# Performance work log

Measured on AMD Instinct MI355X. Metric: run time of the kernel, lower is better.

## Reference

```python
import jax, jax.numpy as jnp
import numpy as np

N = 50000          # nodes
E = 1600000        # edges
IN_C = 128
HID = 128
OUT_C = 1
NUM_LAYERS = 3     # extra conv2 applications
NUM_GRAPHS = 128


def setup_inputs() -> dict:
    key = jax.random.key(0)
    ks = jax.random.split(key, 10)
    x = jax.random.normal(ks[0], (N, IN_C), dtype=jnp.float32)
    edge_index = jax.random.randint(ks[1], (2, E), 0, N, dtype=jnp.int64)
    batch = jnp.sort(jax.random.randint(ks[2], (N,), 0, NUM_GRAPHS, dtype=jnp.int64))
    s1 = 1.0 / np.sqrt(IN_C)
    s2 = 1.0 / np.sqrt(HID)
    W1 = jax.random.uniform(ks[3], (IN_C, HID), jnp.float32, -s1, s1)
    b1 = jnp.zeros((HID,), jnp.float32)
    W2 = jax.random.uniform(ks[4], (HID, HID), jnp.float32, -s2, s2)
    b2 = jnp.zeros((HID,), jnp.float32)
    Wfc = jax.random.uniform(ks[5], (HID, OUT_C), jnp.float32, -s2, s2)
    bfc = jnp.zeros((OUT_C,), jnp.float32)
    return {"x": x, "edge_index": edge_index, "batch": batch,
            "W1": W1, "b1": b1, "W2": W2, "b2": b2, "Wfc": Wfc, "bfc": bfc}


def _gcn_conv(x, W, b, src, dst, dinv):
    # GCNConv: h = X W; out[i] = sum_{j->i} h[j]/sqrt(d_j d_i) + h[i]/d_i + b
    # (self-loops added, symmetric degree normalization, deg includes self-loop)
    h = x @ W                                   # [N, out]
    coef = dinv[src] * dinv[dst]                # [E]
    agg = jax.ops.segment_sum(h[src] * coef[:, None], dst, num_segments=N)
    agg = agg + h * (dinv * dinv)[:, None]      # self-loop contribution
    return agg + b


def reference(x, edge_index, batch, W1, b1, W2, b2, Wfc, bfc):
    src, dst = edge_index[0], edge_index[1]
    # degree of target nodes, +1 for self-loop
    deg = jax.ops.segment_sum(jnp.ones((E,), x.dtype), dst, num_segments=N) + 1.0
    dinv = jax.lax.rsqrt(deg)

    h = jax.nn.relu(_gcn_conv(x, W1, b1, src, dst, dinv))
    for _ in range(NUM_LAYERS):
        h = jax.nn.relu(_gcn_conv(h, W2, b2, src, dst, dinv))
    # dropout is identity here (eval / deterministic reference)

    # global_mean_pool over graphs in the batch
    sums = jax.ops.segment_sum(h, batch, num_segments=NUM_GRAPHS)
    counts = jax.ops.segment_sum(jnp.ones((N,), h.dtype), batch, num_segments=NUM_GRAPHS)
    pooled = sums / jnp.clip(counts, 1.0)[:, None]   # [G, HID]
    return pooled @ Wfc + bfc                        # [G, OUT_C]
```

## Files before the change

### kernel.cpp

```cpp
#include <hip/hip_runtime.h>
#include <hip/hip_bf16.h>


__global__ void count_deg_kernel(const int* __restrict__ dst, int* __restrict__ deg, int E) {
    int i = blockIdx.x * blockDim.x + threadIdx.x;
    int e = i * 4;
    if (e + 3 < E) {
        int4 d = *(const int4*)(dst + e);
        atomicAdd(&deg[d.x], 1);
        atomicAdd(&deg[d.y], 1);
        atomicAdd(&deg[d.z], 1);
        atomicAdd(&deg[d.w], 1);
    } else {
        for (; e < E; e++) atomicAdd(&deg[dst[e]], 1);
    }
}

__global__ void dinv_kernel(const int* __restrict__ deg, float* __restrict__ dinv,
                            float* __restrict__ h0, float* __restrict__ h1,
                            int n, int ns) {
    int i = blockIdx.x * blockDim.x + threadIdx.x;
    if (i < n) dinv[i] = (float)(1.0 / sqrt((double)(deg[i] + 1)));
    if (i < 128) {
        int p = i >> 5, c = i & 31;
        size_t off = (size_t)p * ns * 32 + (size_t)n * 32 + c;
        h0[off] = 0.f;
        h1[off] = 0.f;
    }
}

__global__ void scan_blocksum_kernel(const int* __restrict__ cnt, int* __restrict__ bsum,
                                     int n2) {
    __shared__ int red[256];
    int t = threadIdx.x;
    int i = blockIdx.x * 256 + t;
    red[t] = (i < n2) ? cnt[i] : 0;
    __syncthreads();
    for (int off = 128; off > 0; off >>= 1) {
        if (t < off) red[t] += red[t + off];
        __syncthreads();
    }
    if (t == 0) bsum[blockIdx.x] = red[0];
}

__global__ __launch_bounds__(1024) void scan_bsum_kernel(const int* __restrict__ bsum,
                                                         int* __restrict__ boff, int nb) {
    __shared__ int s[1024];
    int t = threadIdx.x;
    int v = (t < nb) ? bsum[t] : 0;
    s[t] = v;
    __syncthreads();
    for (int off = 1; off < 1024; off <<= 1) {
        int u = (t >= off) ? s[t - off] : 0;
        __syncthreads();
        s[t] += u;
        __syncthreads();
    }
    if (t < nb) boff[t] = s[t] - v;
}

__global__ void scan_final_kernel(const int* __restrict__ cnt, const int* __restrict__ boff,
                                  int* __restrict__ row, int n2) {
    __shared__ int s[256];
    int t = threadIdx.x;
    int b = blockIdx.x;
    int i = b * 256 + t;
    int v = (i < n2) ? cnt[i] : 0;
    s[t] = v;
    __syncthreads();
    for (int off = 1; off < 256; off <<= 1) {
        int u = (t >= off) ? s[t - off] : 0;
        __syncthreads();
        s[t] += u;
        __syncthreads();
    }
    int incl = s[t];
    int base = boff[b];
    if (i < n2) row[i] = base + incl - v;
    if (i == n2 - 1) row[n2] = base + incl;
}

__global__ __launch_bounds__(256) void csr_fill_kernel(const int* __restrict__ src,
                                                       const int* __restrict__ dst,
                                                       const int* __restrict__ row,
                                                       int* __restrict__ fill,
                                                       unsigned short* __restrict__ csr,
                                                       int E, int N) {
    int g  = blockIdx.x & 7;
    int gb = blockIdx.x >> 3;
    int group_blocks = gridDim.x >> 3;
    int R  = (N + 7) >> 3;
    int lo = g * R;
    int hi = lo + R; if (hi > N) hi = N;

    int tig    = gb * blockDim.x + threadIdx.x;
    int stride = group_blocks * blockDim.x;
    int nq = (E + 3) >> 2;

    for (int q = tig; q < nq; q += stride) {
        int e = q * 4;
        if (e + 3 < E) {
            int4 d = *(const int4*)(dst + e);
            if (d.x >= lo && d.x < hi) {
                int pos = row[d.x] + atomicAdd(&fill[d.x], 1);
                csr[pos] = (unsigned short)src[e + 0];
            }
            if (d.y >= lo && d.y < hi) {
                int pos = row[d.y] + atomicAdd(&fill[d.y], 1);
                csr[pos] = (unsigned short)src[e + 1];
            }
            if (d.z >= lo && d.z < hi) {
                int pos = row[d.z] + atomicAdd(&fill[d.z], 1);
                csr[pos] = (unsigned short)src[e + 2];
            }
            if (d.w >= lo && d.w < hi) {
                int pos = row[d.w] + atomicAdd(&fill[d.w], 1);
                csr[pos] = (unsigned short)src[e + 3];
            }
        } else {
            for (; e < E; e++) {
                int d = dst[e];
                if (d >= lo && d < hi) {
                    int pos = row[d] + atomicAdd(&fill[d], 1);
                    csr[pos] = (unsigned short)src[e];
                }
            }
        }
    }
}

__global__ __launch_bounds__(256) void gemm_kernel(const float* __restrict__ A,
                                                   const float* __restrict__ W,
                                                   const float* __restrict__ dinv,
                                                   float* __restrict__ C, int n, int ns,
                                                   int a_blocked) {
    __shared__ float sW[2][16 * 128];
    __shared__ float sA[2][16 * 68];
    int t = threadIdx.x;
    int row0 = blockIdx.x * 64;

    int a_rowi = t >> 2;
    int a_q    = t & 3;
    int w_krow = t >> 4;
    int w_c    = (t & 15) * 8;

    auto a_src = [&](int kb) -> const float* {
        int rr = row0 + a_rowi; if (rr > n - 1) rr = n - 1;
        return a_blocked
            ? (A + ((size_t)(kb >> 1) * ns + rr) * 32 + (kb & 1) * 16 + a_q * 4)
            : (A + (size_t)rr * 128 + kb * 16 + a_q * 4);
    };

    {
        float4 av = *(const float4*)a_src(0);
        float4 w0 = *(const float4*)(W + (size_t)w_krow * 128 + w_c);
        float4 w1 = *(const float4*)(W + (size_t)w_krow * 128 + w_c + 4);
        sA[0][(a_q * 4 + 0) * 68 + a_rowi] = av.x;
        sA[0][(a_q * 4 + 1) * 68 + a_rowi] = av.y;
        sA[0][(a_q * 4 + 2) * 68 + a_rowi] = av.z;
        sA[0][(a_q * 4 + 3) * 68 + a_rowi] = av.w;
        *(float4*)(&sW[0][w_krow * 128 + w_c])     = w0;
        *(float4*)(&sW[0][w_krow * 128 + w_c + 4]) = w1;
    }
    __syncthreads();

    int rg = t >> 4;
    int cg = (t & 15) * 8;

    float acc[4][8];
    #pragma unroll
    for (int j = 0; j < 4; j++)
        #pragma unroll
        for (int c = 0; c < 8; c++) acc[j][c] = 0.f;

    #pragma unroll 1
    for (int kb = 0; kb < 8; kb++) {
        float4 pa, pw0, pw1;
        if (kb < 7) {
            pa  = *(const float4*)a_src(kb + 1);
            pw0 = *(const float4*)(W + (size_t)((kb + 1) * 16 + w_krow) * 128 + w_c);
            pw1 = *(const float4*)(W + (size_t)((kb + 1) * 16 + w_krow) * 128 + w_c + 4);
        }

        const float* ab = sA[kb & 1];
        const float* wb = sW[kb & 1];
        #pragma unroll
        for (int k = 0; k < 16; k++) {
            float4 a4 = *(const float4*)(ab + k * 68 + rg * 4);
            float4 w0 = *(const float4*)(wb + k * 128 + cg);
            float4 w1 = *(const float4*)(wb + k * 128 + cg + 4);
            #pragma unroll
            for (int j = 0; j < 4; j++) {
                float av = (j == 0) ? a4.x : (j == 1) ? a4.y : (j == 2) ? a4.z : a4.w;
                acc[j][0] = fmaf(av, w0.x, acc[j][0]);
                acc[j][1] = fmaf(av, w0.y, acc[j][1]);
                acc[j][2] = fmaf(av, w0.z, acc[j][2]);
                acc[j][3] = fmaf(av, w0.w, acc[j][3]);
                acc[j][4] = fmaf(av, w1.x, acc[j][4]);
                acc[j][5] = fmaf(av, w1.y, acc[j][5]);
                acc[j][6] = fmaf(av, w1.z, acc[j][6]);
                acc[j][7] = fmaf(av, w1.w, acc[j][7]);
            }
        }

        if (kb < 7) {
            int nb = (kb + 1) & 1;
            sA[nb][(a_q * 4 + 0) * 68 + a_rowi] = pa.x;
            sA[nb][(a_q * 4 + 1) * 68 + a_rowi] = pa.y;
            sA[nb][(a_q * 4 + 2) * 68 + a_rowi] = pa.z;
            sA[nb][(a_q * 4 + 3) * 68 + a_rowi] = pa.w;
            *(float4*)(&sW[nb][w_krow * 128 + w_c])     = pw0;
            *(float4*)(&sW[nb][w_krow * 128 + w_c + 4]) = pw1;
        }
        __syncthreads();
    }

    int p  = cg >> 5;
    int cw = cg & 31;
    float* Cb = C + (size_t)p * ns * 32 + cw;
    #pragma unroll
    for (int j = 0; j < 4; j++) {
        int rr = row0 + rg * 4 + j;
        if (rr < n) {
            float dsc = dinv[rr];
            *(float4*)(Cb + (size_t)rr * 32) =
                make_float4(acc[j][0] * dsc, acc[j][1] * dsc,
                            acc[j][2] * dsc, acc[j][3] * dsc);
            *(float4*)(Cb + (size_t)rr * 32 + 4) =
                make_float4(acc[j][4] * dsc, acc[j][5] * dsc,
                            acc[j][6] * dsc, acc[j][7] * dsc);
        }
    }
}

__global__ __launch_bounds__(256) void agg_kernel(const float* __restrict__ h,
                                                  const int* __restrict__ row_ptr,
                                                  const unsigned short* __restrict__ csr,
                                                  const float* __restrict__ dinv,
                                                  const float* __restrict__ bias,
                                                  float* __restrict__ out,
                                                  int n, int ns) {
    int p = blockIdx.x & 3;
    int i = (blockIdx.x >> 2) * 32 + (threadIdx.x >> 3);
    int q = threadIdx.x & 7;
    bool valid = (i < n);
    int iv = valid ? i : 0;

    const float* slice  = h   + (size_t)p * ns * 32;
    float*       oslice = out + (size_t)p * ns * 32;

    int beg = row_ptr[iv];
    int end = valid ? row_ptr[iv + 1] : beg;
    int qoff = q << 2;

    float di = dinv[iv];
    float4 self = *(const float4*)(slice + ((size_t)iv << 5) + qoff);
    float4 b4   = *(const float4*)(bias + p * 32 + qoff);

    float4 acc = make_float4(0.f, 0.f, 0.f, 0.f);

    int e = beg;
    int s0 = (int)__builtin_nontemporal_load(csr + e);
    int s1 = (int)__builtin_nontemporal_load(csr + e + 1);
    int s2 = (int)__builtin_nontemporal_load(csr + e + 2);
    int s3 = (int)__builtin_nontemporal_load(csr + e + 3);
    int s4 = (int)__builtin_nontemporal_load(csr + e + 4);
    int s5 = (int)__builtin_nontemporal_load(csr + e + 5);
    int s6 = (int)__builtin_nontemporal_load(csr + e + 6);
    int s7 = (int)__builtin_nontemporal_load(csr + e + 7);

    while (__any(e < end)) {
        int en = e + 8;
        int t0 = (int)__builtin_nontemporal_load(csr + en);
        int t1 = (int)__builtin_nontemporal_load(csr + en + 1);
        int t2 = (int)__builtin_nontemporal_load(csr + en + 2);
        int t3 = (int)__builtin_nontemporal_load(csr + en + 3);
        int t4 = (int)__builtin_nontemporal_load(csr + en + 4);
        int t5 = (int)__builtin_nontemporal_load(csr + en + 5);
        int t6 = (int)__builtin_nontemporal_load(csr + en + 6);
        int t7 = (int)__builtin_nontemporal_load(csr + en + 7);

        int g0 = (e     < end) ? s0 : n;
        int g1 = (e + 1 < end) ? s1 : n;
        int g2 = (e + 2 < end) ? s2 : n;
        int g3 = (e + 3 < end) ? s3 : n;
        int g4 = (e + 4 < end) ? s4 : n;
        int g5 = (e + 5 < end) ? s5 : n;
        int g6 = (e + 6 < end) ? s6 : n;
        int g7 = (e + 7 < end) ? s7 : n;

        float4 v0 = *(const float4*)(slice + ((size_t)g0 << 5) + qoff);
        float4 v1 = *(const float4*)(slice + ((size_t)g1 << 5) + qoff);
        float4 v2 = *(const float4*)(slice + ((size_t)g2 << 5) + qoff);
        float4 v3 = *(const float4*)(slice + ((size_t)g3 << 5) + qoff);
        float4 v4 = *(const float4*)(slice + ((size_t)g4 << 5) + qoff);
        float4 v5 = *(const float4*)(slice + ((size_t)g5 << 5) + qoff);
        float4 v6 = *(const float4*)(slice + ((size_t)g6 << 5) + qoff);
        float4 v7 = *(const float4*)(slice + ((size_t)g7 << 5) + qoff);

        acc.x += v0.x; acc.y += v0.y; acc.z += v0.z; acc.w += v0.w;
        acc.x += v1.x; acc.y += v1.y; acc.z += v1.z; acc.w += v1.w;
        acc.x += v2.x; acc.y += v2.y; acc.z += v2.z; acc.w += v2.w;
        acc.x += v3.x; acc.y += v3.y; acc.z += v3.z; acc.w += v3.w;
        acc.x += v4.x; acc.y += v4.y; acc.z += v4.z; acc.w += v4.w;
        acc.x += v5.x; acc.y += v5.y; acc.z += v5.z; acc.w += v5.w;
        acc.x += v6.x; acc.y += v6.y; acc.z += v6.z; acc.w += v6.w;
        acc.x += v7.x; acc.y += v7.y; acc.z += v7.z; acc.w += v7.w;

        e = en;
        s0 = t0; s1 = t1; s2 = t2; s3 = t3;
        s4 = t4; s5 = t5; s6 = t6; s7 = t7;
    }

    if (valid) {
        float4 o;
        o.x = fmaxf(fmaf(acc.x + self.x, di, b4.x), 0.f);
        o.y = fmaxf(fmaf(acc.y + self.y, di, b4.y), 0.f);
        o.z = fmaxf(fmaf(acc.z + self.z, di, b4.z), 0.f);
        o.w = fmaxf(fmaf(acc.w + self.w, di, b4.w), 0.f);
        *(float4*)(oslice + ((size_t)i << 5) + qoff) = o;
    }
}

__global__ __launch_bounds__(128) void pool_partial_kernel(const float* __restrict__ h,
                                                           const int* __restrict__ batch,
                                                           double* __restrict__ partials,
                                                           int n, int ns, int S) {
    int g = blockIdx.x / S;
    int s = blockIdx.x % S;
    int c = threadIdx.x;
    const float* hb = h + (size_t)(c >> 5) * ns * 32 + (c & 31);

    int lo = 0, hi = n;
    while (lo < hi) { int mid = (lo + hi) >> 1; if (batch[mid] < g) lo = mid + 1; else hi = mid; }
    int start = lo;
    lo = start; hi = n;
    while (lo < hi) { int mid = (lo + hi) >> 1; if (batch[mid] < g + 1) lo = mid + 1; else hi = mid; }
    int end = lo;

    int cnt = end - start;
    int per = (cnt + S - 1) / S;
    int rs = start + s * per;
    int re = rs + per; if (re > end) re = end;

    double a0 = 0.0, a1 = 0.0, a2 = 0.0, a3 = 0.0;
    int r = rs;
    for (; r + 4 <= re; r += 4) {
        a0 += (double)hb[(size_t)(r + 0) * 32];
        a1 += (double)hb[(size_t)(r + 1) * 32];
        a2 += (double)hb[(size_t)(r + 2) * 32];
        a3 += (double)hb[(size_t)(r + 3) * 32];
    }
    for (; r < re; r++) a0 += (double)hb[(size_t)r * 32];
    partials[(size_t)(g * S + s) * 128 + c] = (a0 + a1) + (a2 + a3);
}

__global__ __launch_bounds__(128) void pool_fc_final_kernel(const double* __restrict__ partials,
                                                            const int* __restrict__ batch,
                                                            const float* __restrict__ Wfc,
                                                            const float* __restrict__ bfc,
                                                            float* __restrict__ out,
                                                            int n, int S) {
    int g = blockIdx.x;
    int c = threadIdx.x;

    int lo = 0, hi = n;
    while (lo < hi) { int mid = (lo + hi) >> 1; if (batch[mid] < g) lo = mid + 1; else hi = mid; }
    int start = lo;
    lo = start; hi = n;
    while (lo < hi) { int mid = (lo + hi) >> 1; if (batch[mid] < g + 1) lo = mid + 1; else hi = mid; }
    int cnt = lo - start;

    double sum = 0.0;
    for (int s = 0; s < S; s++) sum += partials[(size_t)(g * S + s) * 128 + c];
    double mean = sum / (double)(cnt > 0 ? cnt : 1);
    double v = mean * (double)Wfc[c];

    __shared__ double red[128];
    red[c] = v;
    __syncthreads();
    for (int off = 64; off > 0; off >>= 1) {
        if (c < off) red[c] += red[c + off];
        __syncthreads();
    }
    if (c == 0) out[g] = (float)(red[0] + (double)bfc[0]);
}

extern "C" void kernel_launch(void* const* d_in, const int* in_sizes, int n_in,
                              void* d_out, int out_size, void* d_ws, size_t ws_size,
                              hipStream_t stream) {
    const float* x          = (const float*)d_in[0];
    const int*   edge_index = (const int*)d_in[1];
    const int*   batch      = (const int*)d_in[2];
    const float* W1  = (const float*)d_in[3];
    const float* b1  = (const float*)d_in[4];
    const float* W2  = (const float*)d_in[5];
    const float* b2  = (const float*)d_in[6];
    const float* Wfc = (const float*)d_in[7];
    const float* bfc = (const float*)d_in[8];
    float* out = (float*)d_out;

    const int N = in_sizes[2];
    const int E = in_sizes[1] / 2;
    const int G = out_size;
    const int NS = N + 1;

    const int* e_src = edge_index;
    const int* e_dst = edge_index + E;

    char* p = (char*)d_ws;
    auto alloc = [&](size_t bytes) {
        void* r = (void*)p;
        p += (bytes + 255) & ~(size_t)255;
        return r;
    };
    const int S = 8;
    const int NB = (N + 255) / 256;
    float*          h0        = (float*)alloc((size_t)NS * 128 * 4);
    float*          h1        = (float*)alloc((size_t)NS * 128 * 4);
    unsigned short* csr       = (unsigned short*)alloc(((size_t)E + 1024) * 2);
    int*            row       = (int*)  alloc((size_t)(N + 1) * 4);
    int*            deg       = (int*)  alloc((size_t)N * 4);
    int*            fill      = (int*)  alloc((size_t)N * 4);
    int*            bsum      = (int*)  alloc((size_t)NB * 4);
    int*            boff      = (int*)  alloc((size_t)NB * 4);
    float*          dinv      = (float*)alloc((size_t)N * 4);
    double*         partials  = (double*)alloc((size_t)G * S * 128 * 8);
    (void)ws_size; (void)n_in;

    hipMemsetAsync(deg,  0, (size_t)N * 4, stream);
    hipMemsetAsync(fill, 0, (size_t)N * 4, stream);

    int tb = 256;
    int e4 = (E + 3) / 4;
    count_deg_kernel<<<(e4 + tb - 1) / tb, tb, 0, stream>>>(e_dst, deg, E);
    dinv_kernel<<<(N + tb - 1) / tb, tb, 0, stream>>>(deg, dinv, h0, h1, N, NS);
    scan_blocksum_kernel<<<NB, 256, 0, stream>>>(deg, bsum, N);
    scan_bsum_kernel<<<1, 1024, 0, stream>>>(bsum, boff, NB);
    scan_final_kernel<<<NB, 256, 0, stream>>>(deg, boff, row, N);
    csr_fill_kernel<<<1024, tb, 0, stream>>>(e_src, e_dst, row, fill, csr, E, N);

    int gemm_blocks = (N + 63) / 64;
    int agg_blocks  = 4 * ((N + 31) / 32);

    gemm_kernel<<<gemm_blocks, 256, 0, stream>>>(x, W1, dinv, h1, N, NS, 0);
    agg_kernel<<<agg_blocks, 256, 0, stream>>>(h1, row, csr, dinv, b1, h0, N, NS);

    for (int l = 0; l < 3; l++) {
        gemm_kernel<<<gemm_blocks, 256, 0, stream>>>(h0, W2, dinv, h1, N, NS, 1);
        agg_kernel<<<agg_blocks, 256, 0, stream>>>(h1, row, csr, dinv, b2, h0, N, NS);
    }

    pool_partial_kernel<<<G * S, 128, 0, stream>>>(h0, batch, partials, N, NS, S);
    pool_fc_final_kernel<<<G, 128, 0, stream>>>(partials, batch, Wfc, bfc, out, N, S);
}
```

Measured before the change: 711.0 us.

## Record per-edge slot from degree atomics, build CSR without second atomic pass

The degree-count kernel now keeps the value returned by each atomicAdd as the edge's slot within its destination row. The CSR fill becomes a plain scatter with no atomics and no 8-way range partitioning, and the fill buffer and its memset are dropped. The dinv computation and padding-row zeroing move into the scan kernel, removing one launch. Aggregation output now uses nontemporal stores. The cost is an extra E-sized position array that is written and read once, and the CSR order within each row is still nondeterministic.

```diff
diff --git a/kernel.cpp b/kernel.cpp
--- a/kernel.cpp
+++ b/kernel.cpp
@@ -2,30 +2,21 @@
 #include <hip/hip_bf16.h>
 
 
-__global__ void count_deg_kernel(const int* __restrict__ dst, int* __restrict__ deg, int E) {
+typedef float nfloat4 __attribute__((ext_vector_type(4)));
+
+__global__ void count_deg_kernel(const int* __restrict__ dst, int* __restrict__ deg,
+                                 int* __restrict__ pos, int E) {
     int i = blockIdx.x * blockDim.x + threadIdx.x;
     int e = i * 4;
     if (e + 3 < E) {
         int4 d = *(const int4*)(dst + e);
-        atomicAdd(&deg[d.x], 1);
-        atomicAdd(&deg[d.y], 1);
-        atomicAdd(&deg[d.z], 1);
-        atomicAdd(&deg[d.w], 1);
+        int p0 = atomicAdd(&deg[d.x], 1);
+        int p1 = atomicAdd(&deg[d.y], 1);
+        int p2 = atomicAdd(&deg[d.z], 1);
+        int p3 = atomicAdd(&deg[d.w], 1);
+        *(int4*)(pos + e) = make_int4(p0, p1, p2, p3);
     } else {
-        for (; e < E; e++) atomicAdd(&deg[dst[e]], 1);
-    }
-}
-
-__global__ void dinv_kernel(const int* __restrict__ deg, float* __restrict__ dinv,
-                            float* __restrict__ h0, float* __restrict__ h1,
-                            int n, int ns) {
-    int i = blockIdx.x * blockDim.x + threadIdx.x;
-    if (i < n) dinv[i] = (float)(1.0 / sqrt((double)(deg[i] + 1)));
-    if (i < 128) {
-        int p = i >> 5, c = i & 31;
-        size_t off = (size_t)p * ns * 32 + (size_t)n * 32 + c;
-        h0[off] = 0.f;
-        h1[off] = 0.f;
+        for (; e < E; e++) pos[e] = atomicAdd(&deg[dst[e]], 1);
     }
 }
 
@@ -60,7 +51,9 @@
 }
 
 __global__ void scan_final_kernel(const int* __restrict__ cnt, const int* __restrict__ boff,
-                                  int* __restrict__ row, int n2) {
+                                  int* __restrict__ row, float* __restrict__ dinv,
+                                  float* __restrict__ h0, float* __restrict__ h1,
+                                  int n2, int ns) {
     __shared__ int s[256];
     int t = threadIdx.x;
     int b = blockIdx.x;
@@ -76,56 +69,37 @@
     }
     int incl = s[t];
     int base = boff[b];
-    if (i < n2) row[i] = base + incl - v;
+    if (i < n2) {
+        row[i] = base + incl - v;
+        dinv[i] = (float)(1.0 / sqrt((double)(v + 1)));
+    }
     if (i == n2 - 1) row[n2] = base + incl;
+    if (i < 128) {
+        int p = i >> 5, c = i & 31;
+        size_t off2 = (size_t)p * ns * 32 + (size_t)n2 * 32 + c;
+        h0[off2] = 0.f;
+        h1[off2] = 0.f;
+    }
 }
 
 __global__ __launch_bounds__(256) void csr_fill_kernel(const int* __restrict__ src,
                                                        const int* __restrict__ dst,
                                                        const int* __restrict__ row,
-                                                       int* __restrict__ fill,
+                                                       const int* __restrict__ pos,
                                                        unsigned short* __restrict__ csr,
-                                                       int E, int N) {
-    int g  = blockIdx.x & 7;
-    int gb = blockIdx.x >> 3;
-    int group_blocks = gridDim.x >> 3;
-    int R  = (N + 7) >> 3;
-    int lo = g * R;
-    int hi = lo + R; if (hi > N) hi = N;
-
-    int tig    = gb * blockDim.x + threadIdx.x;
-    int stride = group_blocks * blockDim.x;
-    int nq = (E + 3) >> 2;
-
-    for (int q = tig; q < nq; q += stride) {
-        int e = q * 4;
-        if (e + 3 < E) {
-            int4 d = *(const int4*)(dst + e);
-            if (d.x >= lo && d.x < hi) {
-                int pos = row[d.x] + atomicAdd(&fill[d.x], 1);
-                csr[pos] = (unsigned short)src[e + 0];
-            }
-            if (d.y >= lo && d.y < hi) {
-                int pos = row[d.y] + atomicAdd(&fill[d.y], 1);
-                csr[pos] = (unsigned short)src[e + 1];
-            }
-            if (d.z >= lo && d.z < hi) {
-                int pos = row[d.z] + atomicAdd(&fill[d.z], 1);
-                csr[pos] = (unsigned short)src[e + 2];
-            }
-            if (d.w >= lo && d.w < hi) {
-                int pos = row[d.w] + atomicAdd(&fill[d.w], 1);
-                csr[pos] = (unsigned short)src[e + 3];
-            }
-        } else {
-            for (; e < E; e++) {
-                int d = dst[e];
-                if (d >= lo && d < hi) {
-                    int pos = row[d] + atomicAdd(&fill[d], 1);
-                    csr[pos] = (unsigned short)src[e];
-                }
-            }
-        }
+                                                       int E) {
+    int i = blockIdx.x * blockDim.x + threadIdx.x;
+    int e = i * 4;
+    if (e + 3 < E) {
+        int4 d = *(const int4*)(dst + e);
+        int4 s = *(const int4*)(src + e);
+        int4 p = *(const int4*)(pos + e);
+        csr[row[d.x] + p.x] = (unsigned short)s.x;
+        csr[row[d.y] + p.y] = (unsigned short)s.y;
+        csr[row[d.z] + p.z] = (unsigned short)s.z;
+        csr[row[d.w] + p.w] = (unsigned short)s.w;
+    } else {
+        for (; e < E; e++) csr[row[dst[e]] + pos[e]] = (unsigned short)src[e];
     }
 }
 
@@ -313,12 +287,12 @@
     }
 
     if (valid) {
-        float4 o;
+        nfloat4 o;
         o.x = fmaxf(fmaf(acc.x + self.x, di, b4.x), 0.f);
         o.y = fmaxf(fmaf(acc.y + self.y, di, b4.y), 0.f);
         o.z = fmaxf(fmaf(acc.z + self.z, di, b4.z), 0.f);
         o.w = fmaxf(fmaf(acc.w + self.w, di, b4.w), 0.f);
-        *(float4*)(oslice + ((size_t)i << 5) + qoff) = o;
+        __builtin_nontemporal_store(o, (nfloat4*)(oslice + ((size_t)i << 5) + qoff));
     }
 }
 
@@ -421,24 +395,22 @@
     unsigned short* csr       = (unsigned short*)alloc(((size_t)E + 1024) * 2);
     int*            row       = (int*)  alloc((size_t)(N + 1) * 4);
     int*            deg       = (int*)  alloc((size_t)N * 4);
-    int*            fill      = (int*)  alloc((size_t)N * 4);
+    int*            pos       = (int*)  alloc((size_t)(E + 4) * 4);
     int*            bsum      = (int*)  alloc((size_t)NB * 4);
     int*            boff      = (int*)  alloc((size_t)NB * 4);
     float*          dinv      = (float*)alloc((size_t)N * 4);
     double*         partials  = (double*)alloc((size_t)G * S * 128 * 8);
     (void)ws_size; (void)n_in;
 
-    hipMemsetAsync(deg,  0, (size_t)N * 4, stream);
-    hipMemsetAsync(fill, 0, (size_t)N * 4, stream);
+    hipMemsetAsync(deg, 0, (size_t)N * 4, stream);
 
     int tb = 256;
     int e4 = (E + 3) / 4;
-    count_deg_kernel<<<(e4 + tb - 1) / tb, tb, 0, stream>>>(e_dst, deg, E);
-    dinv_kernel<<<(N + tb - 1) / tb, tb, 0, stream>>>(deg, dinv, h0, h1, N, NS);
+    count_deg_kernel<<<(e4 + tb - 1) / tb, tb, 0, stream>>>(e_dst, deg, pos, E);
     scan_blocksum_kernel<<<NB, 256, 0, stream>>>(deg, bsum, N);
     scan_bsum_kernel<<<1, 1024, 0, stream>>>(bsum, boff, NB);
-    scan_final_kernel<<<NB, 256, 0, stream>>>(deg, boff, row, N);
-    csr_fill_kernel<<<1024, tb, 0, stream>>>(e_src, e_dst, row, fill, csr, E, N);
+    scan_final_kernel<<<NB, 256, 0, stream>>>(deg, boff, row, dinv, h0, h1, N, NS);
+    csr_fill_kernel<<<(e4 + tb - 1) / tb, tb, 0, stream>>>(e_src, e_dst, row, pos, csr, E);
 
     int gemm_blocks = (N + 63) / 64;
     int agg_blocks  = 4 * ((N + 31) / 32);
```

New measurement: 659.3 us. 7.3% less time.
